# Kernel tuning notes

Measured on AMD Instinct MI355X. Metric: run time of the kernel, lower is better.

The kernel has to match this reference:

```python
import jax, jax.numpy as jnp
import numpy as np

B = 128
N_IN = 32      # n_inp_capsules
D_IN = 8       # dim_inp_capsules
N_OUT = 10     # n_out_capsules
D_OUT = 16     # dim_out_capsules
DIM = 12       # dim_input (spatial side)
N = N_IN * DIM * DIM  # 4608 total input capsule positions
NUM_ROUTING = 3


def setup_inputs() -> dict:
    key = jax.random.key(0)
    k1, k2 = jax.random.split(key)
    x = jax.random.normal(k1, (B, D_IN, N_IN, DIM, DIM), dtype=jnp.float32)
    weight = jax.random.normal(k2, (D_IN, D_OUT, N, N_OUT), dtype=jnp.float32)
    return {"x": x, "weight": weight}


def squash(s, axis):
    # s_sq/(1+s_sq) * s / sqrt(s_sq)  -- exactly the module's squash (no eps)
    s_sq = jnp.sum(s * s, axis=axis, keepdims=True)
    return s_sq / (1.0 + s_sq) * s / jnp.sqrt(s_sq)


def reference(x, weight):
    b_sz = x.shape[0]
    # view(B, C, -1).permute(0,2,1): (B, N, D_IN)
    u = x.reshape(b_sz, D_IN, -1).transpose(0, 2, 1)
    # u_hat[b,o,n,j] = sum_d u[b,n,d] * weight[d,o,n,j]  (replaces the double python loop)
    u_hat = jnp.einsum('bnd,donj->bonj', u, weight)  # (B, D_OUT, N, N_OUT)
    b = jnp.zeros((b_sz, 1, N, N_OUT), dtype=u_hat.dtype)
    s = None
    for _ in range(NUM_ROUTING):
        c = jax.nn.softmax(b, axis=3)                      # over output capsules
        s = squash(jnp.sum(u_hat * c, axis=2), axis=1)     # (B, D_OUT, N_OUT)
        b = b + jnp.sum(s[:, :, None, :] * u_hat, axis=1, keepdims=True)
    return s  # torch returns s.squeeze() of (B, D_OUT, 1, N_OUT) -> (B, D_OUT, N_OUT)
```

## Files before the change

### kernel.cpp

```cpp
#include <hip/hip_runtime.h>
#include <math.h>

#define NTOT 4608

typedef _Float16 f16;
typedef _Float16 f16x4 __attribute__((ext_vector_type(4)));
typedef _Float16 f16x8 __attribute__((ext_vector_type(8)));
typedef float f32x4 __attribute__((ext_vector_type(4)));
typedef unsigned int u32x2 __attribute__((ext_vector_type(2)));
typedef unsigned int u32x4 __attribute__((ext_vector_type(4)));

__device__ __forceinline__ void nt_store8(void* p, f16x4 v) {
    u32x2 u; __builtin_memcpy(&u, &v, 8);
    __builtin_nontemporal_store(u, (u32x2*)p);
}
__device__ __forceinline__ f16x8 nt_load16(const void* p) {
    u32x4 u = __builtin_nontemporal_load((const u32x4*)p);
    f16x8 v; __builtin_memcpy(&v, &u, 16);
    return v;
}

__global__ __launch_bounds__(320) void prep(const float* __restrict__ x, const float* __restrict__ W,
                                            f16* __restrict__ ut, f16* __restrict__ wt) {
    __shared__ float l[2560];
    const int k = threadIdx.x;
    if (blockIdx.x < 2304) {
        const int n0 = blockIdx.x * 2;
        #pragma unroll
        for (int r = 0; r < 8; ++r) {
            const int f = k + r * 320;
            const int p = f / 20, q = f - p * 20;
            l[f] = W[(size_t)p * 46080 + n0 * 10 + q];
        }
        __syncthreads();
        const int half = k / 160, rr = k - half * 160;
        const int j = rr >> 4, o = rr & 15;
        f16x8 v;
        #pragma unroll
        for (int d = 0; d < 8; ++d)
            v[d] = (f16)l[d * 320 + o * 20 + half * 10 + j];
        *reinterpret_cast<f16x8*>(wt + ((size_t)(n0 + half) * 160 + rr) * 8) = v;
    } else {
        const int t = (blockIdx.x - 2304) * 320 + k;
        if (t < 128 * NTOT) {
            const int b = t / NTOT, n = t - b * NTOT;
            f16x8 v;
            #pragma unroll
            for (int d = 0; d < 8; ++d)
                v[d] = (f16)x[((size_t)b * 8 + d) * NTOT + n];
            *reinterpret_cast<f16x8*>(ut + (size_t)t * 8) = v;
        }
    }
}

__global__ __launch_bounds__(256) void kernelA(const f16* __restrict__ ut, const f16* __restrict__ wt,
                                               f16* __restrict__ uh, float* __restrict__ partial) {
    __shared__ float s0t[4][16][164];
    const int tid = threadIdx.x, w = tid >> 6, lane = tid & 63;
    const int col = lane & 15, qA = lane >> 4;
    const int chunk = blockIdx.x, bg = blockIdx.y, b0 = bg * 16;
    const int b = b0 + col;
    const int nstart = chunk * 32 + w * 8;

    const f16* ab = wt + ((size_t)nstart * 160 + col) * 8;
    const f16* ub = ut + ((size_t)b * NTOT + nstart) * 8;
    f16* uhw = uh + (size_t)nstart * 20480 + (size_t)(qA >> 1) * 1024 + b * 8 + (qA & 1) * 4;

    const f32x4 cz = {0.f, 0.f, 0.f, 0.f};
    f32x4 s0a[10];
    #pragma unroll
    for (int m = 0; m < 10; ++m) s0a[m] = cz;

    for (int nl = 0; nl < 8; ++nl) {
        const f16x8 bf = *reinterpret_cast<const f16x8*>(ub + nl * 8);
        #pragma unroll
        for (int m = 0; m < 10; ++m) {
            const f16x8 af = *reinterpret_cast<const f16x8*>(ab + ((size_t)nl * 160 + m * 16) * 8);
            f32x4 C = __builtin_amdgcn_mfma_f32_16x16x32_f16(af, bf, cz, 0, 0, 0);
            s0a[m] += C;
            f16x4 hv;
            hv[0] = (f16)(0.25f * C[0]); hv[1] = (f16)(0.25f * C[1]);
            hv[2] = (f16)(0.25f * C[2]); hv[3] = (f16)(0.25f * C[3]);
            nt_store8(uhw + (size_t)nl * 20480 + m * 2048, hv);
        }
    }

    #pragma unroll
    for (int m = 0; m < 10; ++m)
        *reinterpret_cast<f32x4*>(&s0t[w][col][m * 16 + qA * 4]) = s0a[m];
    __syncthreads();
    for (int r = tid; r < 2560; r += 256) {
        const int row = r / 160, slot = r - row * 160;
        float v = s0t[0][row][slot] + s0t[1][row][slot] + s0t[2][row][slot] + s0t[3][row][slot];
        partial[((size_t)chunk * 128 + b0 + row) * 160 + slot] = v;
    }
}

__device__ __forceinline__ void kernelB_impl(const f16* __restrict__ uh, const float* __restrict__ Ar,
                                             float* __restrict__ partial, int chunk) {
    __shared__ float s1t[4][16][164];
    const int tid = threadIdx.x, w = tid >> 6, lane = tid & 63;
    const int g = lane & 15, q = lane >> 4;
    const int bg = blockIdx.y;
    const int b = bg * 16 + g;
    const int nstart = chunk * 32 + w * 8;
    const bool qlow = (q < 2);

    float Af[5][8];
    #pragma unroll
    for (int s = 0; s < 5; ++s) {
        f32x4 a0 = *reinterpret_cast<const f32x4*>(Ar + (size_t)b * 160 + (4 * s + q) * 8);
        f32x4 a1 = *reinterpret_cast<const f32x4*>(Ar + (size_t)b * 160 + (4 * s + q) * 8 + 4);
        #pragma unroll
        for (int t = 0; t < 4; ++t) { Af[s][t] = a0[t]; Af[s][4 + t] = a1[t]; }
    }

    float P[5][8];
    #pragma unroll
    for (int s = 0; s < 5; ++s)
        #pragma unroll
        for (int t = 0; t < 8; ++t) P[s][t] = 0.f;

    const f16* uhb = uh + (size_t)nstart * 20480 + (size_t)q * 1024 + b * 8;

    for (int nl = 0; nl < 8; ++nl) {
        f16x8 U[5];
        #pragma unroll
        for (int s = 0; s < 5; ++s)
            U[s] = nt_load16(uhb + (size_t)nl * 20480 + s * 4096);

        float tp[5];
        #pragma unroll
        for (int s = 0; s < 5; ++s) {
            float acc = 0.f;
            #pragma unroll
            for (int t = 0; t < 8; ++t)
                acc = fmaf(Af[s][t], (float)U[s][t], acc);
            tp[s] = acc;
        }

        float tt[10];
        #pragma unroll
        for (int s = 0; s < 5; ++s) {
            float tq = tp[s] + __shfl_xor(tp[s], 16, 64);
            float tr = __shfl_xor(tq, 32, 64);
            tt[2 * s]     = qlow ? tq : tr;
            tt[2 * s + 1] = qlow ? tr : tq;
        }

        float mx = fmaxf(fmaxf(fmaxf(fmaxf(tt[0], tt[1]), fmaxf(tt[2], tt[3])),
                               fmaxf(fmaxf(tt[4], tt[5]), fmaxf(tt[6], tt[7]))),
                         fmaxf(tt[8], tt[9]));
        float c[10], sum = 0.f;
        #pragma unroll
        for (int j = 0; j < 10; ++j) { float e = __expf(tt[j] - mx); c[j] = e; sum += e; }
        const float inv = 1.0f / sum;

        #pragma unroll
        for (int s = 0; s < 5; ++s) {
            const float cm = (qlow ? c[2 * s] : c[2 * s + 1]) * inv;
            #pragma unroll
            for (int t = 0; t < 8; ++t)
                P[s][t] = fmaf(cm, (float)U[s][t], P[s][t]);
        }
    }

    #pragma unroll
    for (int s = 0; s < 5; ++s) {
        const int sg = 4 * s + q;
        f32x4 p0 = {P[s][0], P[s][1], P[s][2], P[s][3]};
        f32x4 p1 = {P[s][4], P[s][5], P[s][6], P[s][7]};
        *reinterpret_cast<f32x4*>(&s1t[w][g][sg * 8])     = p0;
        *reinterpret_cast<f32x4*>(&s1t[w][g][sg * 8 + 4]) = p1;
    }
    __syncthreads();
    for (int r = tid; r < 2560; r += 256) {
        const int row = r / 160, slot = r - row * 160;
        float v = s1t[0][row][slot] + s1t[1][row][slot] + s1t[2][row][slot] + s1t[3][row][slot];
        partial[((size_t)chunk * 128 + bg * 16 + row) * 160 + slot] = v;
    }
}

template<bool DESC>
__global__ __launch_bounds__(256) void kernelB(const f16* __restrict__ uh, const float* __restrict__ Ar,
                                               float* __restrict__ partial) {
    const int chunk = DESC ? (143 - (int)blockIdx.x) : (int)blockIdx.x;
    kernelB_impl(uh, Ar, partial, chunk);
}

template<int MODE>
__global__ __launch_bounds__(320) void reduce_squash(const float* __restrict__ partial,
                                                     float* __restrict__ Ar, float* __restrict__ out,
                                                     float sumscale) {
    const int b = blockIdx.x, jh = blockIdx.y;
    const int k2 = threadIdx.x % 80;
    const int r  = threadIdx.x / 80;
    const int jp = k2 >> 4, o = k2 & 15;
    const int j  = jh * 5 + jp;
    const int slot = j * 16 + o;
    __shared__ float red[4][80];
    __shared__ float srs[80];
    float acc = 0.f;
    for (int c = r; c < 144; c += 4)
        acc += partial[((size_t)c * 128 + b) * 160 + slot];
    red[r][k2] = acc;
    __syncthreads();
    if (r == 0) srs[k2] = (red[0][k2] + red[1][k2] + red[2][k2] + red[3][k2]) * sumscale;
    __syncthreads();
    if (r == 0) {
        float ssq = 0.f;
        #pragma unroll
        for (int oo = 0; oo < 16; ++oo) { float v = srs[jp * 16 + oo]; ssq = fmaf(v, v, ssq); }
        const float s = srs[k2] * ssq / ((1.f + ssq) * sqrtf(ssq));
        if (MODE == 0)      Ar[(size_t)b * 160 + slot] = s;
        else if (MODE == 1) Ar[(size_t)b * 160 + slot] += s;
        else                out[(size_t)b * 160 + o * 10 + j] = s;
    }
}

extern "C" void kernel_launch(void* const* d_in, const int* in_sizes, int n_in,
                              void* d_out, int out_size, void* d_ws, size_t ws_size,
                              hipStream_t stream) {
    const float* x = (const float*)d_in[0];
    const float* W = (const float*)d_in[1];
    float* out = (float*)d_out;

    f16* ut = (f16*)d_ws;
    f16* wt = ut + (size_t)128 * NTOT * 8;
    f16* uh = wt + (size_t)NTOT * 160 * 8;
    float* Ar = (float*)(uh + (size_t)NTOT * 20 * 128 * 8);
    float* partial = Ar + 128 * 160;

    prep<<<2304 + 1844, 320, 0, stream>>>(x, W, ut, wt);

    dim3 gA(144, 8), gRS(128, 2);
    kernelA<<<gA, 256, 0, stream>>>(ut, wt, uh, partial);
    reduce_squash<0><<<gRS, 320, 0, stream>>>(partial, Ar, out, 0.025f);

    kernelB<true ><<<gA, 256, 0, stream>>>(uh, Ar, partial);
    reduce_squash<1><<<gRS, 320, 0, stream>>>(partial, Ar, out, 1.0f);

    kernelB<false><<<gA, 256, 0, stream>>>(uh, Ar, partial);
    reduce_squash<2><<<gRS, 320, 0, stream>>>(partial, Ar, out, 1.0f);
}
```

Measured before the change: 179.8 us.

## Shrink LDS reduction tiles, prefetch u_hat in routing kernel, drop nontemporal hints

```diff
diff --git a/kernel.cpp b/kernel.cpp
--- a/kernel.cpp
+++ b/kernel.cpp
@@ -7,18 +7,6 @@
 typedef _Float16 f16x4 __attribute__((ext_vector_type(4)));
 typedef _Float16 f16x8 __attribute__((ext_vector_type(8)));
 typedef float f32x4 __attribute__((ext_vector_type(4)));
-typedef unsigned int u32x2 __attribute__((ext_vector_type(2)));
-typedef unsigned int u32x4 __attribute__((ext_vector_type(4)));
-
-__device__ __forceinline__ void nt_store8(void* p, f16x4 v) {
-    u32x2 u; __builtin_memcpy(&u, &v, 8);
-    __builtin_nontemporal_store(u, (u32x2*)p);
-}
-__device__ __forceinline__ f16x8 nt_load16(const void* p) {
-    u32x4 u = __builtin_nontemporal_load((const u32x4*)p);
-    f16x8 v; __builtin_memcpy(&v, &u, 16);
-    return v;
-}
 
 __global__ __launch_bounds__(320) void prep(const float* __restrict__ x, const float* __restrict__ W,
                                             f16* __restrict__ ut, f16* __restrict__ wt) {
@@ -55,7 +43,7 @@
 
 __global__ __launch_bounds__(256) void kernelA(const f16* __restrict__ ut, const f16* __restrict__ wt,
                                                f16* __restrict__ uh, float* __restrict__ partial) {
-    __shared__ float s0t[4][16][164];
+    __shared__ float s0t[4][16][84];
     const int tid = threadIdx.x, w = tid >> 6, lane = tid & 63;
     const int col = lane & 15, qA = lane >> 4;
     const int chunk = blockIdx.x, bg = blockIdx.y, b0 = bg * 16;
@@ -81,24 +69,28 @@
             f16x4 hv;
             hv[0] = (f16)(0.25f * C[0]); hv[1] = (f16)(0.25f * C[1]);
             hv[2] = (f16)(0.25f * C[2]); hv[3] = (f16)(0.25f * C[3]);
-            nt_store8(uhw + (size_t)nl * 20480 + m * 2048, hv);
-        }
-    }
-
-    #pragma unroll
-    for (int m = 0; m < 10; ++m)
-        *reinterpret_cast<f32x4*>(&s0t[w][col][m * 16 + qA * 4]) = s0a[m];
-    __syncthreads();
-    for (int r = tid; r < 2560; r += 256) {
-        const int row = r / 160, slot = r - row * 160;
-        float v = s0t[0][row][slot] + s0t[1][row][slot] + s0t[2][row][slot] + s0t[3][row][slot];
-        partial[((size_t)chunk * 128 + b0 + row) * 160 + slot] = v;
+            *reinterpret_cast<f16x4*>(uhw + (size_t)nl * 20480 + m * 2048) = hv;
+        }
+    }
+
+    #pragma unroll
+    for (int t2 = 0; t2 < 2; ++t2) {
+        #pragma unroll
+        for (int m = 0; m < 5; ++m)
+            *reinterpret_cast<f32x4*>(&s0t[w][col][m * 16 + qA * 4]) = s0a[t2 * 5 + m];
+        __syncthreads();
+        for (int r = tid; r < 1280; r += 256) {
+            const int row = r / 80, Sl = r - row * 80;
+            float v = s0t[0][row][Sl] + s0t[1][row][Sl] + s0t[2][row][Sl] + s0t[3][row][Sl];
+            partial[((size_t)chunk * 128 + b0 + row) * 160 + t2 * 80 + Sl] = v;
+        }
+        if (t2 == 0) __syncthreads();
     }
 }
 
 __device__ __forceinline__ void kernelB_impl(const f16* __restrict__ uh, const float* __restrict__ Ar,
                                              float* __restrict__ partial, int chunk) {
-    __shared__ float s1t[4][16][164];
+    __shared__ float s1t[4][16][100];
     const int tid = threadIdx.x, w = tid >> 6, lane = tid & 63;
     const int g = lane & 15, q = lane >> 4;
     const int bg = blockIdx.y;
@@ -123,11 +115,18 @@
 
     const f16* uhb = uh + (size_t)nstart * 20480 + (size_t)q * 1024 + b * 8;
 
+    f16x8 U[5], V[5];
+    #pragma unroll
+    for (int s = 0; s < 5; ++s)
+        U[s] = *reinterpret_cast<const f16x8*>(uhb + s * 4096);
+
+    #pragma unroll
     for (int nl = 0; nl < 8; ++nl) {
-        f16x8 U[5];
-        #pragma unroll
-        for (int s = 0; s < 5; ++s)
-            U[s] = nt_load16(uhb + (size_t)nl * 20480 + s * 4096);
+        if (nl < 7) {
+            #pragma unroll
+            for (int s = 0; s < 5; ++s)
+                V[s] = *reinterpret_cast<const f16x8*>(uhb + (size_t)(nl + 1) * 20480 + s * 4096);
+        }
 
         float tp[5];
         #pragma unroll
@@ -163,21 +162,41 @@
             for (int t = 0; t < 8; ++t)
                 P[s][t] = fmaf(cm, (float)U[s][t], P[s][t]);
         }
-    }
-
-    #pragma unroll
-    for (int s = 0; s < 5; ++s) {
-        const int sg = 4 * s + q;
+
+        if (nl < 7) {
+            #pragma unroll
+            for (int s = 0; s < 5; ++s) U[s] = V[s];
+        }
+    }
+
+    #pragma unroll
+    for (int s = 0; s < 2; ++s) {
+        const int S = (4 * s + q) * 8;
         f32x4 p0 = {P[s][0], P[s][1], P[s][2], P[s][3]};
         f32x4 p1 = {P[s][4], P[s][5], P[s][6], P[s][7]};
-        *reinterpret_cast<f32x4*>(&s1t[w][g][sg * 8])     = p0;
-        *reinterpret_cast<f32x4*>(&s1t[w][g][sg * 8 + 4]) = p1;
-    }
-    __syncthreads();
-    for (int r = tid; r < 2560; r += 256) {
-        const int row = r / 160, slot = r - row * 160;
-        float v = s1t[0][row][slot] + s1t[1][row][slot] + s1t[2][row][slot] + s1t[3][row][slot];
-        partial[((size_t)chunk * 128 + bg * 16 + row) * 160 + slot] = v;
+        *reinterpret_cast<f32x4*>(&s1t[w][g][S])     = p0;
+        *reinterpret_cast<f32x4*>(&s1t[w][g][S + 4]) = p1;
+    }
+    __syncthreads();
+    for (int r = tid; r < 1024; r += 256) {
+        const int row = r >> 6, Sl = r & 63;
+        float v = s1t[0][row][Sl] + s1t[1][row][Sl] + s1t[2][row][Sl] + s1t[3][row][Sl];
+        partial[((size_t)chunk * 128 + bg * 16 + row) * 160 + Sl] = v;
+    }
+    __syncthreads();
+    #pragma unroll
+    for (int s = 2; s < 5; ++s) {
+        const int S = (4 * (s - 2) + q) * 8;
+        f32x4 p0 = {P[s][0], P[s][1], P[s][2], P[s][3]};
+        f32x4 p1 = {P[s][4], P[s][5], P[s][6], P[s][7]};
+        *reinterpret_cast<f32x4*>(&s1t[w][g][S])     = p0;
+        *reinterpret_cast<f32x4*>(&s1t[w][g][S + 4]) = p1;
+    }
+    __syncthreads();
+    for (int r = tid; r < 1536; r += 256) {
+        const int row = r / 96, Sl = r - row * 96;
+        float v = s1t[0][row][Sl] + s1t[1][row][Sl] + s1t[2][row][Sl] + s1t[3][row][Sl];
+        partial[((size_t)chunk * 128 + bg * 16 + row) * 160 + 64 + Sl] = v;
     }
 }
 
```

New measurement: 213.5 us. 1.19x slower.

## Enlarge per-block n chunk, drop nontemporal hints and softmax max subtraction

Applied to the files above, without the earlier changes.

```diff
diff --git a/kernel.cpp b/kernel.cpp
--- a/kernel.cpp
+++ b/kernel.cpp
@@ -2,23 +2,14 @@
 #include <math.h>
 
 #define NTOT 4608
+#define NCH  96
+#define NPC  48
+#define NPW  12
 
 typedef _Float16 f16;
 typedef _Float16 f16x4 __attribute__((ext_vector_type(4)));
 typedef _Float16 f16x8 __attribute__((ext_vector_type(8)));
 typedef float f32x4 __attribute__((ext_vector_type(4)));
-typedef unsigned int u32x2 __attribute__((ext_vector_type(2)));
-typedef unsigned int u32x4 __attribute__((ext_vector_type(4)));
-
-__device__ __forceinline__ void nt_store8(void* p, f16x4 v) {
-    u32x2 u; __builtin_memcpy(&u, &v, 8);
-    __builtin_nontemporal_store(u, (u32x2*)p);
-}
-__device__ __forceinline__ f16x8 nt_load16(const void* p) {
-    u32x4 u = __builtin_nontemporal_load((const u32x4*)p);
-    f16x8 v; __builtin_memcpy(&v, &u, 16);
-    return v;
-}
 
 __global__ __launch_bounds__(320) void prep(const float* __restrict__ x, const float* __restrict__ W,
                                             f16* __restrict__ ut, f16* __restrict__ wt) {
@@ -60,7 +51,7 @@
     const int col = lane & 15, qA = lane >> 4;
     const int chunk = blockIdx.x, bg = blockIdx.y, b0 = bg * 16;
     const int b = b0 + col;
-    const int nstart = chunk * 32 + w * 8;
+    const int nstart = chunk * NPC + w * NPW;
 
     const f16* ab = wt + ((size_t)nstart * 160 + col) * 8;
     const f16* ub = ut + ((size_t)b * NTOT + nstart) * 8;
@@ -71,7 +62,7 @@
     #pragma unroll
     for (int m = 0; m < 10; ++m) s0a[m] = cz;
 
-    for (int nl = 0; nl < 8; ++nl) {
+    for (int nl = 0; nl < NPW; ++nl) {
         const f16x8 bf = *reinterpret_cast<const f16x8*>(ub + nl * 8);
         #pragma unroll
         for (int m = 0; m < 10; ++m) {
@@ -81,7 +72,7 @@
             f16x4 hv;
             hv[0] = (f16)(0.25f * C[0]); hv[1] = (f16)(0.25f * C[1]);
             hv[2] = (f16)(0.25f * C[2]); hv[3] = (f16)(0.25f * C[3]);
-            nt_store8(uhw + (size_t)nl * 20480 + m * 2048, hv);
+            *reinterpret_cast<f16x4*>(uhw + (size_t)nl * 20480 + m * 2048) = hv;
         }
     }
 
@@ -103,7 +94,7 @@
     const int g = lane & 15, q = lane >> 4;
     const int bg = blockIdx.y;
     const int b = bg * 16 + g;
-    const int nstart = chunk * 32 + w * 8;
+    const int nstart = chunk * NPC + w * NPW;
     const bool qlow = (q < 2);
 
     float Af[5][8];
@@ -123,11 +114,12 @@
 
     const f16* uhb = uh + (size_t)nstart * 20480 + (size_t)q * 1024 + b * 8;
 
-    for (int nl = 0; nl < 8; ++nl) {
+    #pragma unroll
+    for (int nl = 0; nl < NPW; ++nl) {
         f16x8 U[5];
         #pragma unroll
         for (int s = 0; s < 5; ++s)
-            U[s] = nt_load16(uhb + (size_t)nl * 20480 + s * 4096);
+            U[s] = *reinterpret_cast<const f16x8*>(uhb + (size_t)nl * 20480 + s * 4096);
 
         float tp[5];
         #pragma unroll
@@ -148,12 +140,9 @@
             tt[2 * s + 1] = qlow ? tr : tq;
         }
 
-        float mx = fmaxf(fmaxf(fmaxf(fmaxf(tt[0], tt[1]), fmaxf(tt[2], tt[3])),
-                               fmaxf(fmaxf(tt[4], tt[5]), fmaxf(tt[6], tt[7]))),
-                         fmaxf(tt[8], tt[9]));
         float c[10], sum = 0.f;
         #pragma unroll
-        for (int j = 0; j < 10; ++j) { float e = __expf(tt[j] - mx); c[j] = e; sum += e; }
+        for (int j = 0; j < 10; ++j) { float e = __expf(tt[j]); c[j] = e; sum += e; }
         const float inv = 1.0f / sum;
 
         #pragma unroll
@@ -167,11 +156,11 @@
 
     #pragma unroll
     for (int s = 0; s < 5; ++s) {
-        const int sg = 4 * s + q;
+        const int S = (4 * s + q) * 8;
         f32x4 p0 = {P[s][0], P[s][1], P[s][2], P[s][3]};
         f32x4 p1 = {P[s][4], P[s][5], P[s][6], P[s][7]};
-        *reinterpret_cast<f32x4*>(&s1t[w][g][sg * 8])     = p0;
-        *reinterpret_cast<f32x4*>(&s1t[w][g][sg * 8 + 4]) = p1;
+        *reinterpret_cast<f32x4*>(&s1t[w][g][S])     = p0;
+        *reinterpret_cast<f32x4*>(&s1t[w][g][S + 4]) = p1;
     }
     __syncthreads();
     for (int r = tid; r < 2560; r += 256) {
@@ -182,9 +171,10 @@
 }
 
 template<bool DESC>
-__global__ __launch_bounds__(256) void kernelB(const f16* __restrict__ uh, const float* __restrict__ Ar,
-                                               float* __restrict__ partial) {
-    const int chunk = DESC ? (143 - (int)blockIdx.x) : (int)blockIdx.x;
+__global__ __launch_bounds__(256, 3) void kernelB(const f16* __restrict__ uh,
+                                                  const float* __restrict__ Ar,
+                                                  float* __restrict__ partial) {
+    const int chunk = DESC ? (NCH - 1 - (int)blockIdx.x) : (int)blockIdx.x;
     kernelB_impl(uh, Ar, partial, chunk);
 }
 
@@ -201,7 +191,7 @@
     __shared__ float red[4][80];
     __shared__ float srs[80];
     float acc = 0.f;
-    for (int c = r; c < 144; c += 4)
+    for (int c = r; c < NCH; c += 4)
         acc += partial[((size_t)c * 128 + b) * 160 + slot];
     red[r][k2] = acc;
     __syncthreads();
@@ -233,7 +223,7 @@
 
     prep<<<2304 + 1844, 320, 0, stream>>>(x, W, ut, wt);
 
-    dim3 gA(144, 8), gRS(128, 2);
+    dim3 gA(NCH, 8), gRS(128, 2);
     kernelA<<<gA, 256, 0, stream>>>(ut, wt, uh, partial);
     reduce_squash<0><<<gRS, 320, 0, stream>>>(partial, Ar, out, 0.025f);
 
```

Result: slower. 461.8 us (+156.8%).
